# Optimization experiments

Measured on AMD Instinct MI355X. Metric: run time of the kernel, lower is better.

Reference implementation:

```python
import jax, jax.numpy as jnp
import numpy as np

B, LC, LPV, LTP, V, H, NGLO, PREF = 64, 512, 16, 16, 8192, 1024, 30000, 16
BOS = 2
TAU = 0.67
NEG = -1e9


def mask_via_len(lens, max_len):
    # [B,1,max_len] float mask, 1 where pos < len
    return (jnp.arange(max_len)[None, :] < lens[:, None]).astype(jnp.float32)[:, None, :]


def setup_inputs() -> dict:
    key = jax.random.key(0)
    ks = jax.random.split(key, 24)
    s = 0.02
    return {
        "context": jax.random.randint(ks[0], (B, LC), 0, NGLO),
        "context_len": jax.random.randint(ks[1], (B,), 1, LC),
        "pv_m": jax.random.uniform(ks[2], (B, LPV, V), dtype=jnp.float32),
        "pv_m_mask": jnp.ones((B, 1, LPV), jnp.float32),
        "ar_gth": jax.random.randint(ks[3], (B, 1), 0, V),
        "ar_gth_len": jnp.ones((B,), jnp.int64 if jax.config.jax_enable_x64 else jnp.int32),
        "tp_path": jax.random.randint(ks[4], (B, LTP), 0, V),
        "tp_path_len": jax.random.randint(ks[5], (B,), 1, LTP),
        "tp_path_hidden": jax.random.normal(ks[6], (B, LTP, H), jnp.float32),
        "ar_hidden": jax.random.normal(ks[7], (B, 1, H), jnp.float32),
        # learned parameters
        "E_ctx": jax.random.normal(ks[8], (NGLO, H), jnp.float32) * s,
        "W_p": jax.random.normal(ks[9], (V, H), jnp.float32) * s,
        "E_topic": jax.random.normal(ks[10], (V, H), jnp.float32) * s,
        "W_q": jax.random.normal(ks[11], (H, H), jnp.float32) * s,
        "W_k": jax.random.normal(ks[12], (H, H), jnp.float32) * s,
        "W_v": jax.random.normal(ks[13], (H, H), jnp.float32) * s,
        "W_o": jax.random.normal(ks[14], (H, H), jnp.float32) * s,
        "gen_W": jax.random.normal(ks[15], (H, V), jnp.float32) * s,
        "gen_b": jnp.zeros((V,), jnp.float32),
        "glo2loc": jax.random.randint(ks[16], (NGLO,), 0, V),
    }


def _decode(seq_gumbel, src_hidden, src_mask, E_topic, W_q, W_k, W_v, W_o):
    # single-step cross-attention decoder stand-in; dec_out [B,1,H]
    emb = seq_gumbel[:, -1:, :] @ E_topic                      # [B,1,H]
    q = emb @ W_q
    k = src_hidden @ W_k
    v = src_hidden @ W_v
    s = jnp.einsum("bqh,bsh->bqs", q, k) * (H ** -0.5)
    s = jnp.where(src_mask == 0, NEG, s)                       # src_mask [B,1,Ls]
    a = jax.nn.softmax(s, axis=-1)
    ctx = jnp.einsum("bqs,bsh->bqh", a, v)
    return jnp.tanh((emb + ctx) @ W_o)


def _proj(dec_out, src_hidden, src_mask, pv_m, transfer_ctx, tp_oh, gen_W, gen_b):
    # dec_out [B,1,H]
    bsz = dec_out.shape[0]
    gen_logit = dec_out @ gen_W + gen_b                        # [B,1,V]
    hid = src_hidden[:, :-1, :]
    msk = src_mask[:, :, :-1]                                  # [B,1,Ls-1]
    copy_logit = jnp.einsum("bqh,bsh->bqs", dec_out, hid)
    copy_logit = jnp.where(msk == 0, NEG, copy_logit)
    logits = jnp.concatenate([gen_logit, copy_logit], -1) * (H ** -0.5)  # scale_prj
    probs = jax.nn.softmax(logits, axis=-1)
    gen_prob = probs[:, :, :V]
    copy_ctx_p = probs[:, :, V:V + LC]
    copy_pv_p = probs[:, :, V + LC:V + LC + LPV] @ pv_m        # [B,1,V]
    copy_tp_p = probs[:, :, V + LC + LPV:V + LC + LPV + LTP] @ tp_oh
    # scatter-add context copy mass into local topic vocab
    ccopy = jnp.zeros((bsz, 1, V), probs.dtype)
    ccopy = ccopy.at[jnp.arange(bsz)[:, None, None], 0, transfer_ctx[:, None, :]].add(copy_ctx_p)
    return gen_prob + copy_pv_p + copy_tp_p + ccopy


def reference(context, context_len, pv_m, pv_m_mask, ar_gth, ar_gth_len, tp_path,
              tp_path_len, tp_path_hidden, ar_hidden, E_ctx, W_p, E_topic,
              W_q, W_k, W_v, W_o, gen_W, gen_b, glo2loc):
    ar_mask = mask_via_len(ar_gth_len, 1)
    ctx_mask = mask_via_len(context_len, LC)
    ctx_hidden = E_ctx[context] * jnp.swapaxes(ctx_mask, 1, 2)  # masked-embedding encoder
    pv_hidden = jnp.einsum("blv,vh->blh", pv_m, W_p)            # p_encoder stand-in
    tp_oh = jax.nn.one_hot(tp_path, V, dtype=jnp.float32)
    tp_mask = mask_via_len(tp_path_len, LTP)
    src_hidden = jnp.concatenate([ctx_hidden, pv_hidden, tp_path_hidden, ar_hidden], 1)
    src_mask = jnp.concatenate([ctx_mask, pv_m_mask, tp_mask, ar_mask], 2)
    transfer_ctx = glo2loc[context]                             # [B,LC] -> topic vocab ids

    seq = jax.nn.one_hot(jnp.full((pv_m.shape[0], 1), BOS), V, dtype=jnp.float32)
    probs_steps = []
    gkey = jax.random.key(42)
    for t in range(PREF):
        dec = _decode(jax.lax.stop_gradient(seq), src_hidden, src_mask,
                      E_topic, W_q, W_k, W_v, W_o)
        p = _proj(dec, src_hidden, src_mask, pv_m, transfer_ctx, tp_oh, gen_W, gen_b)
        # gumbel-softmax on normed probs
        u = jax.random.uniform(jax.random.fold_in(gkey, t), p.shape, minval=1e-10, maxval=1.0)
        g = -jnp.log(-jnp.log(u))
        y = jax.nn.softmax((jnp.log(p + 1e-10) + g) / TAU, axis=-1)
        probs_steps.append(p)
        seq = jnp.concatenate([seq, y], 1)
    seq_gen_prob = jnp.concatenate(probs_steps, 1)              # [B,PREF,V]
    return seq_gen_prob, seq[:, 1:, :]
```

## Files before the change

kernel.cpp:

```cpp
#include <hip/hip_runtime.h>
#include <hip/hip_bf16.h>
#include <stdint.h>

#define B_    64
#define LC_   512
#define V_    8192
#define H_    1024
#define PREF_ 16
#define S_    545
#define SP_   560
#define NEGV  (-1e9f)
#define INV32 0.03125f

typedef __attribute__((ext_vector_type(8))) short s8v;
typedef __attribute__((ext_vector_type(4))) float f4a;

__device__ __forceinline__ short f2bf(float f){
  uint32_t u = __float_as_uint(f);
  uint32_t r = (u + 0x7fffu + ((u >> 16) & 1u)) >> 16;
  return (short)(r & 0xffffu);
}
__device__ __forceinline__ float bf2f(short s){
  return __uint_as_float(((uint32_t)(uint16_t)s) << 16);
}

__device__ __forceinline__ uint32_t rotl32(uint32_t x, uint32_t d){ return (x<<d)|(x>>(32u-d)); }
__device__ __forceinline__ void tf2x32(uint32_t k0, uint32_t k1, uint32_t& x0, uint32_t& x1){
  uint32_t ks0=k0, ks1=k1, ks2=k0^k1^0x1BD11BDAu;
  x0+=ks0; x1+=ks1;
  x0+=x1; x1=rotl32(x1,13); x1^=x0;
  x0+=x1; x1=rotl32(x1,15); x1^=x0;
  x0+=x1; x1=rotl32(x1,26); x1^=x0;
  x0+=x1; x1=rotl32(x1, 6); x1^=x0;
  x0+=ks1; x1+=ks2+1u;
  x0+=x1; x1=rotl32(x1,17); x1^=x0;
  x0+=x1; x1=rotl32(x1,29); x1^=x0;
  x0+=x1; x1=rotl32(x1,16); x1^=x0;
  x0+=x1; x1=rotl32(x1,24); x1^=x0;
  x0+=ks2; x1+=ks0+2u;
  x0+=x1; x1=rotl32(x1,13); x1^=x0;
  x0+=x1; x1=rotl32(x1,15); x1^=x0;
  x0+=x1; x1=rotl32(x1,26); x1^=x0;
  x0+=x1; x1=rotl32(x1, 6); x1^=x0;
  x0+=ks0; x1+=ks1+3u;
  x0+=x1; x1=rotl32(x1,17); x1^=x0;
  x0+=x1; x1=rotl32(x1,29); x1^=x0;
  x0+=x1; x1=rotl32(x1,16); x1^=x0;
  x0+=x1; x1=rotl32(x1,24); x1^=x0;
  x0+=ks1; x1+=ks2+4u;
  x0+=x1; x1=rotl32(x1,13); x1^=x0;
  x0+=x1; x1=rotl32(x1,15); x1^=x0;
  x0+=x1; x1=rotl32(x1,26); x1^=x0;
  x0+=x1; x1=rotl32(x1, 6); x1^=x0;
  x0+=ks2; x1+=ks0+5u;
}

__global__ __launch_bounds__(256) void cast_bf(const float* __restrict__ in, short* __restrict__ out){
  size_t idx = ((size_t)blockIdx.x*256 + threadIdx.x)*4;
  float4 v = *(const float4*)(in+idx);
  short4 s; s.x=f2bf(v.x); s.y=f2bf(v.y); s.z=f2bf(v.z); s.w=f2bf(v.w);
  *(short4*)(out+idx) = s;
}
__global__ __launch_bounds__(256) void cast_pack(const float* __restrict__ in, short* __restrict__ out, int N){
  int gid = blockIdx.x*256 + threadIdx.x;
  int k = gid / (N>>2);
  int n = (gid % (N>>2))*4;
  float4 v = *(const float4*)(in + (size_t)k*N + n);
  size_t base = ((size_t)(k>>3)*N + n)*8 + (k&7);
  out[base] = f2bf(v.x); out[base+8] = f2bf(v.y); out[base+16] = f2bf(v.z); out[base+24] = f2bf(v.w);
}
__global__ __launch_bounds__(256) void embcast(const float* __restrict__ emb, short* __restrict__ EA){
  int idx = blockIdx.x*256 + threadIdx.x;
  int row = idx >> 8, c4 = idx & 255;
  float4 v = ((const float4*)(emb + (size_t)row*1024))[c4];
  short4 s; s.x=f2bf(v.x); s.y=f2bf(v.y); s.z=f2bf(v.z); s.w=f2bf(v.w);
  *(short4*)(EA + (size_t)row*2048 + c4*4) = s;
}

template<int BM, bool ATOMIC, bool BIAS>
__global__ __launch_bounds__(256) void bgemm(
    const short* __restrict__ A, int lda,
    const short* __restrict__ Bp, int ldn,
    float* __restrict__ C, int ldc,
    int kchunk, const float* __restrict__ bias)
{
  constexpr int BN = 128, BK = 64;
  __shared__ short Bl[BK*BN];
  const int t = threadIdx.x;
  const int w = t >> 6, lane = t & 63;
  const int quad = lane >> 4, l16 = lane & 15;
  const int col0 = blockIdx.x * BN;
  const int row0 = (BM==128) ? blockIdx.y * BM : 0;
  const int k0 = blockIdx.z * kchunk, kend = k0 + kchunk;
  constexpr int MT = 2;
  constexpr int NT = (BM==128) ? 8 : 4;
  const int mbase = (BM==128) ? w*32 : (w&1)*32;
  const int nbase = (BM==128) ? 0 : (w>>1)*64;
  f4a acc[MT][NT];
  #pragma unroll
  for (int mt=0; mt<MT; mt++)
    #pragma unroll
    for (int nt=0; nt<NT; nt++)
      acc[mt][nt] = (f4a){0.f,0.f,0.f,0.f};

  for (int kb = k0; kb < kend; kb += BK){
    #pragma unroll
    for (int i=0;i<4;i++){
      int idx = t + i*256;
      int p = idx >> 7, n = idx & 127;
      ((s8v*)Bl)[idx] = *(const s8v*)(Bp + (((size_t)((kb>>3)+p))*ldn + col0 + n)*8);
    }
    __syncthreads();
    #pragma unroll
    for (int ks=0; ks<BK; ks+=32){
      const int kk = kb + ks + quad*8;
      const int kl = ks + quad*8;
      s8v af[MT], bfr[NT];
      #pragma unroll
      for (int mt=0; mt<MT; mt++)
        af[mt] = *(const s8v*)(A + (size_t)(row0+mbase+mt*16+l16)*lda + kk);
      #pragma unroll
      for (int nt=0; nt<NT; nt++)
        bfr[nt] = *(const s8v*)&Bl[((kl>>3)*BN + nbase + nt*16 + l16)*8];
      #pragma unroll
      for (int mt=0; mt<MT; mt++)
        #pragma unroll
        for (int nt=0; nt<NT; nt++)
          acc[mt][nt] = __builtin_amdgcn_mfma_f32_16x16x32_bf16(af[mt], bfr[nt], acc[mt][nt], 0, 0, 0);
    }
    __syncthreads();
  }
  #pragma unroll
  for (int mt=0; mt<MT; mt++){
    #pragma unroll
    for (int nt=0; nt<NT; nt++){
      #pragma unroll
      for (int r=0; r<4; r++){
        int row = row0 + mbase + mt*16 + quad*4 + r;
        int cc  = col0 + nbase + nt*16 + l16;
        float v = acc[mt][nt][r];
        if (BIAS){ if (!ATOMIC || blockIdx.z==0) v += bias[cc]; }
        size_t idx = (size_t)row*ldc + cc;
        if (ATOMIC) atomicAdd(&C[idx], v);
        else        C[idx] = v;
      }
    }
  }
}

template<bool TRANSB, bool PACK>
__global__ __launch_bounds__(256) void mgemm(
    const float* __restrict__ A, int lda,
    const float* __restrict__ Bm, int ldb,
    float* __restrict__ C, int ldc, int K)
{
  constexpr int BM = 128, BN = 128, BK = 64;
  __shared__ short Ap[BK*BM];
  __shared__ short Bp[BK*BN];
  const int t = threadIdx.x;
  const int w = t >> 6, lane = t & 63;
  const int quad = lane >> 4, l16 = lane & 15;
  const int col0 = blockIdx.x * BN;
  const int row0 = blockIdx.y * BM;
  constexpr int MT = 2, NT = 8;
  const int mbase = w*32, nbase = 0;
  f4a acc[MT][NT];
  #pragma unroll
  for (int mt=0; mt<MT; mt++)
    #pragma unroll
    for (int nt=0; nt<NT; nt++)
      acc[mt][nt] = (f4a){0.f,0.f,0.f,0.f};

  for (int kb = 0; kb < K; kb += BK){
    #pragma unroll
    for (int i = 0; i < 8; ++i){
      int idx = t + i*256;
      int m = idx >> 4, kq = (idx & 15) * 4;
      float4 a = *(const float4*)(A + (size_t)(row0+m)*lda + kb + kq);
      short4 s4; s4.x=f2bf(a.x); s4.y=f2bf(a.y); s4.z=f2bf(a.z); s4.w=f2bf(a.w);
      *(short4*)&Ap[((kq>>3)*BM + m)*8 + (kq&7)] = s4;
    }
    if (TRANSB){
      #pragma unroll
      for (int i = 0; i < 8; ++i){
        int idx = t + i*256;
        int n = idx >> 4, kq = (idx & 15) * 4;
        float4 bv = *(const float4*)(Bm + (size_t)(col0+n)*ldb + kb + kq);
        short4 s4; s4.x=f2bf(bv.x); s4.y=f2bf(bv.y); s4.z=f2bf(bv.z); s4.w=f2bf(bv.w);
        *(short4*)&Bp[((kq>>3)*BN + n)*8 + (kq&7)] = s4;
      }
    } else {
      #pragma unroll
      for (int c = 0; c < 8; ++c){
        int idx = t + c*256;
        int n = idx & 127, kq = (idx >> 7) * 4;
        const float* bp0 = Bm + (size_t)(kb+kq)*ldb + col0 + n;
        float b0 = bp0[0], b1 = bp0[ldb], b2 = bp0[2*(size_t)ldb], b3 = bp0[3*(size_t)ldb];
        short4 s4; s4.x=f2bf(b0); s4.y=f2bf(b1); s4.z=f2bf(b2); s4.w=f2bf(b3);
        *(short4*)&Bp[((kq>>3)*BN + n)*8 + (kq&7)] = s4;
      }
    }
    __syncthreads();
    #pragma unroll
    for (int ks = 0; ks < BK; ks += 32){
      const int kk = ks + quad*8;
      s8v af[MT], bfr[NT];
      #pragma unroll
      for (int mt=0; mt<MT; mt++)
        af[mt] = *(const s8v*)&Ap[((kk>>3)*BM + mbase + mt*16 + l16)*8];
      #pragma unroll
      for (int nt=0; nt<NT; nt++)
        bfr[nt] = *(const s8v*)&Bp[((kk>>3)*BN + nbase + nt*16 + l16)*8];
      #pragma unroll
      for (int mt=0; mt<MT; mt++)
        #pragma unroll
        for (int nt=0; nt<NT; nt++)
          acc[mt][nt] = __builtin_amdgcn_mfma_f32_16x16x32_bf16(af[mt], bfr[nt], acc[mt][nt], 0, 0, 0);
    }
    __syncthreads();
  }
  #pragma unroll
  for (int mt=0; mt<MT; mt++){
    #pragma unroll
    for (int nt=0; nt<NT; nt++){
      #pragma unroll
      for (int r=0; r<4; r++){
        int row = row0 + mbase + mt*16 + quad*4 + r;
        int cc  = col0 + nbase + nt*16 + l16;
        float v = acc[mt][nt][r];
        if (PACK){
          size_t off = (((size_t)(row>>3))*ldc + cc)*8 + (row&7);
          ((short*)C)[off] = f2bf(v);
        } else {
          C[(size_t)row*ldc + cc] = v;
        }
      }
    }
  }
}

__global__ __launch_bounds__(256) void src_build(
    const float* __restrict__ E_ctx, const int* __restrict__ context, const int* __restrict__ ctx_len,
    const float* __restrict__ pvh, const float* __restrict__ pv_mask,
    const float* __restrict__ tp_hidden, const int* __restrict__ tp_len,
    const float* __restrict__ ar_hidden, const int* __restrict__ ar_len,
    short* __restrict__ src, float* __restrict__ smask)
{
  const int b = blockIdx.x, t = threadIdx.x;
  const int j = blockIdx.y*2 + (t >> 7);
  const int c = (t & 127) * 8;
  const float* srcp = nullptr;
  float msk = 0.f;
  if (j < 512){
    bool on = j < ctx_len[b];
    msk = on ? 1.f : 0.f;
    if (on) srcp = E_ctx + (size_t)context[b*LC_ + j]*H_;
  } else if (j < 528){
    srcp = pvh + (size_t)(b*16 + j-512)*H_;
    msk = pv_mask[b*16 + j-512];
  } else if (j < 544){
    srcp = tp_hidden + (size_t)(b*16 + j-528)*H_;
    msk = ((j-528) < tp_len[b]) ? 1.f : 0.f;
  } else if (j == 544){
    srcp = ar_hidden + (size_t)b*H_;
    msk = (ar_len[b] > 0) ? 1.f : 0.f;
  }
  if (srcp){
    float4 v0 = *(const float4*)(srcp + c);
    float4 v1 = *(const float4*)(srcp + c + 4);
    s8v s;
    s[0]=f2bf(v0.x); s[1]=f2bf(v0.y); s[2]=f2bf(v0.z); s[3]=f2bf(v0.w);
    s[4]=f2bf(v1.x); s[5]=f2bf(v1.y); s[6]=f2bf(v1.z); s[7]=f2bf(v1.w);
    *(s8v*)(src + (size_t)(b*SP_ + j)*H_ + c) = s;
  }
  if ((t & 127) == 0) smask[b*SP_ + j] = msk;
}

__global__ __launch_bounds__(256) void abuf_init(short* __restrict__ Abuf){
  int v = blockIdx.x*256 + threadIdx.x;
  int b = blockIdx.y;
  Abuf[(size_t)b*V_ + v] = (v == 2) ? (short)0x3F80 : (short)0;
}

__global__ __launch_bounds__(256) void attn_pass(
    const float* __restrict__ qk, const short* __restrict__ src, const float* __restrict__ smask,
    float* __restrict__ part_o, float* __restrict__ part_ml)
{
  const int b = blockIdx.x, c = blockIdx.y, t = threadIdx.x;
  const int w = t>>6, lane = t&63;
  __shared__ float sv[35], pr[35], red[4];
  float qreg[16];
  {
    const float4* q4 = (const float4*)(qk + (size_t)b*H_ + lane*16);
    #pragma unroll
    for (int i=0;i<4;i++){ float4 v = q4[i]; qreg[4*i]=v.x; qreg[4*i+1]=v.y; qreg[4*i+2]=v.z; qreg[4*i+3]=v.w; }
  }
  const int j0 = c*35;
  for (int r = w; r < 35; r += 4){
    float msk = smask[b*SP_ + j0 + r];
    float s = -3.4e38f;
    if (msk != 0.f){
      const s8v* rp = (const s8v*)(src + (size_t)(b*SP_ + j0 + r)*H_);
      s8v v0 = rp[lane*2], v1 = rp[lane*2+1];
      float acc = 0.f;
      #pragma unroll
      for (int i=0;i<8;i++) acc += bf2f(v0[i])*qreg[i];
      #pragma unroll
      for (int i=0;i<8;i++) acc += bf2f(v1[i])*qreg[8+i];
      #pragma unroll
      for (int off=32; off; off>>=1) acc += __shfl_down(acc, off, 64);
      s = acc * INV32;
    }
    if (lane == 0) sv[r] = s;
  }
  __syncthreads();
  float lm = (t < 35) ? sv[t] : -3.4e38f;
  #pragma unroll
  for (int off=32; off; off>>=1) lm = fmaxf(lm, __shfl_down(lm, off, 64));
  if (lane==0) red[w] = lm;
  __syncthreads();
  const float m = fmaxf(fmaxf(red[0],red[1]), fmaxf(red[2],red[3]));
  __syncthreads();
  if (t < 35) pr[t] = (sv[t] > -1e37f) ? expf(sv[t]-m) : 0.f;
  __syncthreads();
  float ls = (t < 35) ? pr[t] : 0.f;
  #pragma unroll
  for (int off=32; off; off>>=1) ls += __shfl_down(ls, off, 64);
  if (lane==0) red[w] = ls;
  __syncthreads();
  const float lsum = red[0]+red[1]+red[2]+red[3];
  float4 o = {0.f,0.f,0.f,0.f};
  const short* base = src + (size_t)(b*SP_ + j0)*H_ + t*4;
  for (int r=0;r<35;r++){
    float p_ = pr[r];
    if (p_ != 0.f){
      short4 s4 = *(const short4*)(base + (size_t)r*H_);
      o.x += p_*bf2f(s4.x); o.y += p_*bf2f(s4.y); o.z += p_*bf2f(s4.z); o.w += p_*bf2f(s4.w);
    }
  }
  ((float4*)(part_o + (size_t)(b*16+c)*H_))[t] = o;
  if (t==0){ part_ml[(b*16+c)*2] = m; part_ml[(b*16+c)*2+1] = lsum; }
}

__global__ __launch_bounds__(256) void attn_combine(
    const float* __restrict__ part_o, const float* __restrict__ part_ml,
    short* __restrict__ EA)
{
  const int b = blockIdx.x, t = threadIdx.x;
  __shared__ float sm[16], sl[16];
  if (t < 16){ sm[t] = part_ml[(b*16+t)*2]; sl[t] = part_ml[(b*16+t)*2+1]; }
  __syncthreads();
  float M = -3.4e38f;
  #pragma unroll
  for (int i=0;i<16;i++) M = fmaxf(M, sm[i]);
  float wgt[16]; float Z = 0.f;
  #pragma unroll
  for (int i=0;i<16;i++){ wgt[i] = expf(sm[i]-M); Z += wgt[i]*sl[i]; }
  float4 o = {0.f,0.f,0.f,0.f};
  #pragma unroll
  for (int i=0;i<16;i++){
    float4 p = ((const float4*)(part_o + (size_t)(b*16+i)*H_))[t];
    o.x += wgt[i]*p.x; o.y += wgt[i]*p.y; o.z += wgt[i]*p.z; o.w += wgt[i]*p.w;
  }
  float inv = 1.f / Z;
  short4 s4; s4.x=f2bf(o.x*inv); s4.y=f2bf(o.y*inv); s4.z=f2bf(o.z*inv); s4.w=f2bf(o.w*inv);
  *(short4*)(EA + (size_t)b*2048 + 1024 + t*4) = s4;
}

__global__ __launch_bounds__(256) void tanhcast(const float* __restrict__ decr, short* __restrict__ dtan){
  int idx = blockIdx.x*256 + threadIdx.x;
  float4 v = ((const float4*)decr)[idx];
  short4 s; s.x=f2bf(tanhf(v.x)); s.y=f2bf(tanhf(v.y)); s.z=f2bf(tanhf(v.z)); s.w=f2bf(tanhf(v.w));
  ((short4*)dtan)[idx] = s;
}

__global__ __launch_bounds__(256) void copy_score(
    const short* __restrict__ dtan, const short* __restrict__ src, const float* __restrict__ smask,
    float* __restrict__ cl)
{
  const int b = blockIdx.x, c = blockIdx.y, t = threadIdx.x;
  const int w = t>>6, lane = t&63;
  float qd[16];
  {
    const s8v* d8 = (const s8v*)(dtan + (size_t)b*H_ + lane*16);
    s8v d0 = d8[0], d1 = d8[1];
    #pragma unroll
    for (int i=0;i<8;i++){ qd[i] = bf2f(d0[i]); qd[8+i] = bf2f(d1[i]); }
  }
  for (int r = w; r < 34; r += 4){
    int j = c*34 + r;
    float msk = smask[b*SP_ + j];
    float s;
    if (msk != 0.f){
      const s8v* rp = (const s8v*)(src + (size_t)(b*SP_ + j)*H_);
      s8v v0 = rp[lane*2], v1 = rp[lane*2+1];
      float acc = 0.f;
      #pragma unroll
      for (int i=0;i<8;i++) acc += bf2f(v0[i])*qd[i];
      #pragma unroll
      for (int i=0;i<8;i++) acc += bf2f(v1[i])*qd[8+i];
      #pragma unroll
      for (int off=32; off; off>>=1) acc += __shfl_down(acc, off, 64);
      s = acc * INV32;
    } else s = NEGV * INV32;
    if (lane == 0) cl[b*544 + j] = s;
  }
}

__global__ __launch_bounds__(1024) void fuse_out(
    const float* __restrict__ gen, const float* __restrict__ cl, const float* __restrict__ pv_m,
    const int* __restrict__ context, const int* __restrict__ glo2loc, const int* __restrict__ tp_path,
    float* __restrict__ out0, float* __restrict__ out1, short* __restrict__ Abuf, int step)
{
  const int b = blockIdx.x, t = threadIdx.x;
  const int w = t>>6, lane = t&63;
  __shared__ float pl[V_];
  __shared__ float red[16];
  __shared__ float pvp[16];
  float4 gv[2];
  const float4* g4 = (const float4*)(gen + (size_t)b*V_);
  float lm = -3.4e38f;
  #pragma unroll
  for (int i=0;i<2;i++){
    float4 g = g4[t + 1024*i];
    g.x*=INV32; g.y*=INV32; g.z*=INV32; g.w*=INV32;
    gv[i] = g;
    lm = fmaxf(lm, fmaxf(fmaxf(g.x,g.y), fmaxf(g.z,g.w)));
  }
  if (t < 544) lm = fmaxf(lm, cl[b*544+t]);
  #pragma unroll
  for (int off=32; off; off>>=1) lm = fmaxf(lm, __shfl_down(lm, off, 64));
  if (lane==0) red[w] = lm;
  __syncthreads();
  float m = red[0];
  #pragma unroll
  for (int i=1;i<16;i++) m = fmaxf(m, red[i]);
  __syncthreads();
  float ls = 0.f;
  #pragma unroll
  for (int i=0;i<2;i++){
    gv[i].x = expf(gv[i].x - m); gv[i].y = expf(gv[i].y - m);
    gv[i].z = expf(gv[i].z - m); gv[i].w = expf(gv[i].w - m);
    ls += gv[i].x + gv[i].y + gv[i].z + gv[i].w;
  }
  if (t < 544) ls += expf(cl[b*544+t] - m);
  #pragma unroll
  for (int off=32; off; off>>=1) ls += __shfl_down(ls, off, 64);
  if (lane==0) red[w] = ls;
  __syncthreads();
  float Z = red[0];
  #pragma unroll
  for (int i=1;i<16;i++) Z += red[i];
  const float invZ = 1.f / Z;
  if (t < 16) pvp[t] = expf(cl[b*544 + 512 + t] - m) * invZ;
  __syncthreads();
  #pragma unroll
  for (int i=0;i<2;i++){ gv[i].x*=invZ; gv[i].y*=invZ; gv[i].z*=invZ; gv[i].w*=invZ; }
  for (int l=0;l<16;l++){
    float wl = pvp[l];
    const float4* pv4 = (const float4*)(pv_m + (size_t)(b*16+l)*V_);
    #pragma unroll
    for (int i=0;i<2;i++){
      float4 q = pv4[t + 1024*i];
      gv[i].x += wl*q.x; gv[i].y += wl*q.y; gv[i].z += wl*q.z; gv[i].w += wl*q.w;
    }
  }
  #pragma unroll
  for (int i=0;i<2;i++) ((float4*)pl)[t + 1024*i] = gv[i];
  __syncthreads();
  if (t < 528){
    float val; int tgt;
    if (t < 512){
      val = expf(cl[b*544 + t] - m) * invZ;
      tgt = glo2loc[context[b*LC_ + t]];
    } else {
      int l = t - 512;
      val = expf(cl[b*544 + 528 + l] - m) * invZ;
      tgt = tp_path[b*16 + l];
    }
    if (val != 0.f) atomicAdd(&pl[tgt], val);
  }
  __syncthreads();
  float* o0 = out0 + (size_t)(b*PREF_+step)*V_;
  uint32_t kx = 0u, ky = (uint32_t)step;
  tf2x32(0u, 42u, kx, ky);
  float lv[8];
  float lm2 = -3.4e38f;
  #pragma unroll
  for (int i=0;i<2;i++){
    float4 p4 = ((const float4*)pl)[t + 1024*i];
    ((float4*)o0)[t + 1024*i] = p4;
    float pe[4] = {p4.x, p4.y, p4.z, p4.w};
    #pragma unroll
    for (int k=0;k<4;k++){
      int v = 4*(t + 1024*i) + k;
      uint32_t j = (uint32_t)(b*V_ + v);
      uint32_t x0 = 0u, x1 = j;
      tf2x32(kx, ky, x0, x1);
      uint32_t bits = x0 ^ x1;
      float f = __uint_as_float((bits >> 9) | 0x3F800000u) - 1.0f;
      float u = fmaxf(1e-10f, f + 1e-10f);
      float g = -logf(-logf(u));
      float l = (logf(pe[k] + 1e-10f) + g) / 0.67f;
      lv[4*i+k] = l;
      lm2 = fmaxf(lm2, l);
    }
  }
  #pragma unroll
  for (int off=32; off; off>>=1) lm2 = fmaxf(lm2, __shfl_down(lm2, off, 64));
  if (lane==0) red[w] = lm2;
  __syncthreads();
  float m2 = red[0];
  #pragma unroll
  for (int i=1;i<16;i++) m2 = fmaxf(m2, red[i]);
  __syncthreads();
  float ls2 = 0.f;
  #pragma unroll
  for (int i=0;i<8;i++){ lv[i] = expf(lv[i] - m2); ls2 += lv[i]; }
  #pragma unroll
  for (int off=32; off; off>>=1) ls2 += __shfl_down(ls2, off, 64);
  if (lane==0) red[w] = ls2;
  __syncthreads();
  float Z2 = red[0];
  #pragma unroll
  for (int i=1;i<16;i++) Z2 += red[i];
  float* y = out1 + (size_t)(b*PREF_ + step)*V_;
  short* ab = Abuf + (size_t)b*V_;
  #pragma unroll
  for (int i=0;i<2;i++){
    float4 y4; y4.x = lv[4*i]/Z2; y4.y = lv[4*i+1]/Z2; y4.z = lv[4*i+2]/Z2; y4.w = lv[4*i+3]/Z2;
    ((float4*)y)[t + 1024*i] = y4;
    short4 s4; s4.x=f2bf(y4.x); s4.y=f2bf(y4.y); s4.z=f2bf(y4.z); s4.w=f2bf(y4.w);
    *(short4*)(ab + 4*(t + 1024*i)) = s4;
  }
}

extern "C" void kernel_launch(void* const* d_in, const int* in_sizes, int n_in,
                              void* d_out, int out_size, void* d_ws, size_t ws_size,
                              hipStream_t stream)
{
  (void)in_sizes; (void)n_in; (void)out_size; (void)ws_size;
  const int*   context   = (const int*)  d_in[0];
  const int*   ctx_len   = (const int*)  d_in[1];
  const float* pv_m      = (const float*)d_in[2];
  const float* pv_mask   = (const float*)d_in[3];
  const int*   ar_len    = (const int*)  d_in[5];
  const int*   tp_path   = (const int*)  d_in[6];
  const int*   tp_len    = (const int*)  d_in[7];
  const float* tp_hidden = (const float*)d_in[8];
  const float* ar_hidden = (const float*)d_in[9];
  const float* E_ctx     = (const float*)d_in[10];
  const float* W_p       = (const float*)d_in[11];
  const float* E_topic   = (const float*)d_in[12];
  const float* W_q       = (const float*)d_in[13];
  const float* W_k       = (const float*)d_in[14];
  const float* W_v       = (const float*)d_in[15];
  const float* W_o       = (const float*)d_in[16];
  const float* gen_W     = (const float*)d_in[17];
  const float* gen_b     = (const float*)d_in[18];
  const int*   glo2loc   = (const int*)  d_in[19];

  float* out0 = (float*)d_out;
  float* out1 = out0 + (size_t)B_*PREF_*V_;

  short* sw      = (short*)d_ws;
  short* Etp_pk  = sw;  sw += (size_t)8192*1024;
  short* genW_pk = sw;  sw += (size_t)1024*8192;
  short* WoV_pk  = sw;  sw += (size_t)2048*1024;
  short* Mw_pk   = sw;  sw += (size_t)1024*1024;
  short* Abuf    = sw;  sw += (size_t)B_*V_;
  short* EA      = sw;  sw += (size_t)B_*2048;
  short* dtan    = sw;  sw += (size_t)B_*H_;
  short* src_bf  = sw;  sw += (size_t)B_*SP_*H_;
  short* pvm_bf  = src_bf;
  short* Wp_pk   = src_bf + (size_t)1024*8192;
  float* fw      = (float*)sw;
  float* smask   = fw;  fw += B_*SP_;
  float* pvh     = fw;  fw += 1024*1024;
  float* emb     = fw;  fw += B_*H_;
  float* qk      = fw;  fw += B_*H_;
  float* decr    = fw;  fw += B_*H_;
  float* gen     = fw;  fw += (size_t)B_*V_;
  float* part_o  = fw;  fw += (size_t)B_*16*H_;
  float* part_ml = fw;  fw += B_*16*2;
  float* cl      = fw;  fw += B_*544;
  const size_t zbytes = (size_t)(3*B_*H_) * sizeof(float);

  hipMemsetAsync(pvh, 0, (size_t)1024*1024*sizeof(float), stream);
  cast_bf  <<<dim3(8192), dim3(256), 0, stream>>>(pv_m, pvm_bf);
  cast_pack<<<dim3(8192), dim3(256), 0, stream>>>(W_p, Wp_pk, 1024);
  bgemm<128,true,false><<<dim3(8,8,4), dim3(256), 0, stream>>>(
      pvm_bf, 8192, Wp_pk, 1024, pvh, 1024, 2048, nullptr);
  mgemm<true,true><<<dim3(8,8,1), dim3(256), 0, stream>>>(
      W_q, H_, W_k, H_, (float*)Mw_pk, H_, H_);
  cast_pack<<<dim3(1024), dim3(256), 0, stream>>>(W_o, WoV_pk, 1024);
  mgemm<false,true><<<dim3(8,8,1), dim3(256), 0, stream>>>(
      W_v, H_, W_o, H_, (float*)(WoV_pk + (size_t)1024*1024), H_, H_);
  cast_pack<<<dim3(8192), dim3(256), 0, stream>>>(E_topic, Etp_pk, 1024);
  cast_pack<<<dim3(8192), dim3(256), 0, stream>>>(gen_W, genW_pk, 8192);
  src_build<<<dim3(64,280), dim3(256), 0, stream>>>(
      E_ctx, context, ctx_len, pvh, pv_mask, tp_hidden, tp_len, ar_hidden, ar_len, src_bf, smask);
  abuf_init<<<dim3(32,64), dim3(256), 0, stream>>>(Abuf);

  for (int t = 0; t < PREF_; ++t){
    hipMemsetAsync(emb, 0, zbytes, stream);
    bgemm<64,true,false><<<dim3(8,1,16), dim3(256), 0, stream>>>(
        Abuf, V_, Etp_pk, H_, emb, H_, 512, nullptr);
    embcast<<<dim3(64), dim3(256), 0, stream>>>(emb, EA);
    bgemm<64,true,false><<<dim3(8,1,2), dim3(256), 0, stream>>>(
        EA, 2048, Mw_pk, H_, qk, H_, 512, nullptr);
    attn_pass<<<dim3(64,16), dim3(256), 0, stream>>>(qk, src_bf, smask, part_o, part_ml);
    attn_combine<<<dim3(64), dim3(256), 0, stream>>>(part_o, part_ml, EA);
    bgemm<64,true,false><<<dim3(8,1,4), dim3(256), 0, stream>>>(
        EA, 2048, WoV_pk, H_, decr, H_, 512, nullptr);
    tanhcast<<<dim3(64), dim3(256), 0, stream>>>(decr, dtan);
    bgemm<64,false,true><<<dim3(64,1,1), dim3(256), 0, stream>>>(
        dtan, H_, genW_pk, V_, gen, V_, 1024, gen_b);
    copy_score<<<dim3(64,16), dim3(256), 0, stream>>>(dtan, src_bf, smask, cl);
    fuse_out<<<dim3(64), dim3(1024), 0, stream>>>(
        gen, cl, pv_m, context, glo2loc, tp_path, out0, out1, Abuf, t);
  }
}
```

Baseline: 2.720 ms.

## Double-buffer bgemm B tiles, replace mgemm with bf16 bgemm, read bf16 pv_m

The bgemm kernel now double-buffers its shared-memory B tile, loading the next K tile while computing the current one. The fp32 mgemm weight-fusion GEMMs are replaced by bf16 casts followed by split-K bgemm with a repack step. The per-step Mw and WoV GEMVs get more K splits. fuse_out now reads the bf16 pv_m copy kept in its own buffer instead of fp32 pv_m, with 8 contiguous elements per thread. This trades extra shared memory, more atomics and a bit of bf16 precision loss in the pv mixture for less memory traffic and better latency hiding.

Result: faster. 2.217 ms (-18.5%).

```diff
diff --git a/kernel.cpp b/kernel.cpp
--- a/kernel.cpp
+++ b/kernel.cpp
@@ -69,6 +69,15 @@
   size_t base = ((size_t)(k>>3)*N + n)*8 + (k&7);
   out[base] = f2bf(v.x); out[base+8] = f2bf(v.y); out[base+16] = f2bf(v.z); out[base+24] = f2bf(v.w);
 }
+__global__ __launch_bounds__(256) void cast_packT(const float* __restrict__ in, short* __restrict__ out, int N, int K){
+  int gid = blockIdx.x*256 + threadIdx.x;
+  int n = gid / (K>>2);
+  int k = (gid % (K>>2))*4;
+  float4 v = *(const float4*)(in + (size_t)n*K + k);
+  size_t base = ((size_t)(k>>3)*N + n)*8 + (k&7);
+  short4 s4; s4.x=f2bf(v.x); s4.y=f2bf(v.y); s4.z=f2bf(v.z); s4.w=f2bf(v.w);
+  *(short4*)(out + base) = s4;
+}
 __global__ __launch_bounds__(256) void embcast(const float* __restrict__ emb, short* __restrict__ EA){
   int idx = blockIdx.x*256 + threadIdx.x;
   int row = idx >> 8, c4 = idx & 255;
@@ -85,13 +94,14 @@
     int kchunk, const float* __restrict__ bias)
 {
   constexpr int BN = 128, BK = 64;
-  __shared__ short Bl[BK*BN];
+  __shared__ short Bl[2][BK*BN];
   const int t = threadIdx.x;
   const int w = t >> 6, lane = t & 63;
   const int quad = lane >> 4, l16 = lane & 15;
   const int col0 = blockIdx.x * BN;
   const int row0 = (BM==128) ? blockIdx.y * BM : 0;
-  const int k0 = blockIdx.z * kchunk, kend = k0 + kchunk;
+  const int k0 = blockIdx.z * kchunk;
+  const int nk = kchunk / BK;
   constexpr int MT = 2;
   constexpr int NT = (BM==128) ? 8 : 4;
   const int mbase = (BM==128) ? w*32 : (w&1)*32;
@@ -103,14 +113,21 @@
     for (int nt=0; nt<NT; nt++)
       acc[mt][nt] = (f4a){0.f,0.f,0.f,0.f};
 
-  for (int kb = k0; kb < kend; kb += BK){
+  auto stage = [&](int kb, int buf){
     #pragma unroll
     for (int i=0;i<4;i++){
       int idx = t + i*256;
       int p = idx >> 7, n = idx & 127;
-      ((s8v*)Bl)[idx] = *(const s8v*)(Bp + (((size_t)((kb>>3)+p))*ldn + col0 + n)*8);
-    }
-    __syncthreads();
+      ((s8v*)Bl[buf])[idx] = *(const s8v*)(Bp + (((size_t)((kb>>3)+p))*ldn + col0 + n)*8);
+    }
+  };
+
+  stage(k0, 0);
+  __syncthreads();
+  for (int it=0; it<nk; ++it){
+    const int kb = k0 + it*BK;
+    const int cur = it & 1;
+    if (it+1 < nk) stage(kb + BK, cur^1);
     #pragma unroll
     for (int ks=0; ks<BK; ks+=32){
       const int kk = kb + ks + quad*8;
@@ -121,7 +138,7 @@
         af[mt] = *(const s8v*)(A + (size_t)(row0+mbase+mt*16+l16)*lda + kk);
       #pragma unroll
       for (int nt=0; nt<NT; nt++)
-        bfr[nt] = *(const s8v*)&Bl[((kl>>3)*BN + nbase + nt*16 + l16)*8];
+        bfr[nt] = *(const s8v*)&Bl[cur][((kl>>3)*BN + nbase + nt*16 + l16)*8];
       #pragma unroll
       for (int mt=0; mt<MT; mt++)
         #pragma unroll
@@ -143,97 +160,6 @@
         size_t idx = (size_t)row*ldc + cc;
         if (ATOMIC) atomicAdd(&C[idx], v);
         else        C[idx] = v;
-      }
-    }
-  }
-}
-
-template<bool TRANSB, bool PACK>
-__global__ __launch_bounds__(256) void mgemm(
-    const float* __restrict__ A, int lda,
-    const float* __restrict__ Bm, int ldb,
-    float* __restrict__ C, int ldc, int K)
-{
-  constexpr int BM = 128, BN = 128, BK = 64;
-  __shared__ short Ap[BK*BM];
-  __shared__ short Bp[BK*BN];
-  const int t = threadIdx.x;
-  const int w = t >> 6, lane = t & 63;
-  const int quad = lane >> 4, l16 = lane & 15;
-  const int col0 = blockIdx.x * BN;
-  const int row0 = blockIdx.y * BM;
-  constexpr int MT = 2, NT = 8;
-  const int mbase = w*32, nbase = 0;
-  f4a acc[MT][NT];
-  #pragma unroll
-  for (int mt=0; mt<MT; mt++)
-    #pragma unroll
-    for (int nt=0; nt<NT; nt++)
-      acc[mt][nt] = (f4a){0.f,0.f,0.f,0.f};
-
-  for (int kb = 0; kb < K; kb += BK){
-    #pragma unroll
-    for (int i = 0; i < 8; ++i){
-      int idx = t + i*256;
-      int m = idx >> 4, kq = (idx & 15) * 4;
-      float4 a = *(const float4*)(A + (size_t)(row0+m)*lda + kb + kq);
-      short4 s4; s4.x=f2bf(a.x); s4.y=f2bf(a.y); s4.z=f2bf(a.z); s4.w=f2bf(a.w);
-      *(short4*)&Ap[((kq>>3)*BM + m)*8 + (kq&7)] = s4;
-    }
-    if (TRANSB){
-      #pragma unroll
-      for (int i = 0; i < 8; ++i){
-        int idx = t + i*256;
-        int n = idx >> 4, kq = (idx & 15) * 4;
-        float4 bv = *(const float4*)(Bm + (size_t)(col0+n)*ldb + kb + kq);
-        short4 s4; s4.x=f2bf(bv.x); s4.y=f2bf(bv.y); s4.z=f2bf(bv.z); s4.w=f2bf(bv.w);
-        *(short4*)&Bp[((kq>>3)*BN + n)*8 + (kq&7)] = s4;
-      }
-    } else {
-      #pragma unroll
-      for (int c = 0; c < 8; ++c){
-        int idx = t + c*256;
-        int n = idx & 127, kq = (idx >> 7) * 4;
-        const float* bp0 = Bm + (size_t)(kb+kq)*ldb + col0 + n;
-        float b0 = bp0[0], b1 = bp0[ldb], b2 = bp0[2*(size_t)ldb], b3 = bp0[3*(size_t)ldb];
-        short4 s4; s4.x=f2bf(b0); s4.y=f2bf(b1); s4.z=f2bf(b2); s4.w=f2bf(b3);
-        *(short4*)&Bp[((kq>>3)*BN + n)*8 + (kq&7)] = s4;
-      }
-    }
-    __syncthreads();
-    #pragma unroll
-    for (int ks = 0; ks < BK; ks += 32){
-      const int kk = ks + quad*8;
-      s8v af[MT], bfr[NT];
-      #pragma unroll
-      for (int mt=0; mt<MT; mt++)
-        af[mt] = *(const s8v*)&Ap[((kk>>3)*BM + mbase + mt*16 + l16)*8];
-      #pragma unroll
-      for (int nt=0; nt<NT; nt++)
-        bfr[nt] = *(const s8v*)&Bp[((kk>>3)*BN + nbase + nt*16 + l16)*8];
-      #pragma unroll
-      for (int mt=0; mt<MT; mt++)
-        #pragma unroll
-        for (int nt=0; nt<NT; nt++)
-          acc[mt][nt] = __builtin_amdgcn_mfma_f32_16x16x32_bf16(af[mt], bfr[nt], acc[mt][nt], 0, 0, 0);
-    }
-    __syncthreads();
-  }
-  #pragma unroll
-  for (int mt=0; mt<MT; mt++){
-    #pragma unroll
-    for (int nt=0; nt<NT; nt++){
-      #pragma unroll
-      for (int r=0; r<4; r++){
-        int row = row0 + mbase + mt*16 + quad*4 + r;
-        int cc  = col0 + nbase + nt*16 + l16;
-        float v = acc[mt][nt][r];
-        if (PACK){
-          size_t off = (((size_t)(row>>3))*ldc + cc)*8 + (row&7);
-          ((short*)C)[off] = f2bf(v);
-        } else {
-          C[(size_t)row*ldc + cc] = v;
-        }
       }
     }
   }
@@ -408,7 +334,7 @@
 }
 
 __global__ __launch_bounds__(1024) void fuse_out(
-    const float* __restrict__ gen, const float* __restrict__ cl, const float* __restrict__ pv_m,
+    const float* __restrict__ gen, const float* __restrict__ cl, const short* __restrict__ pvm,
     const int* __restrict__ context, const int* __restrict__ glo2loc, const int* __restrict__ tp_path,
     float* __restrict__ out0, float* __restrict__ out1, short* __restrict__ Abuf, int step)
 {
@@ -417,15 +343,15 @@
   __shared__ float pl[V_];
   __shared__ float red[16];
   __shared__ float pvp[16];
-  float4 gv[2];
+  float ge[8];
   const float4* g4 = (const float4*)(gen + (size_t)b*V_);
   float lm = -3.4e38f;
-  #pragma unroll
-  for (int i=0;i<2;i++){
-    float4 g = g4[t + 1024*i];
-    g.x*=INV32; g.y*=INV32; g.z*=INV32; g.w*=INV32;
-    gv[i] = g;
-    lm = fmaxf(lm, fmaxf(fmaxf(g.x,g.y), fmaxf(g.z,g.w)));
+  {
+    float4 ga = g4[2*t], gb = g4[2*t+1];
+    ge[0]=ga.x*INV32; ge[1]=ga.y*INV32; ge[2]=ga.z*INV32; ge[3]=ga.w*INV32;
+    ge[4]=gb.x*INV32; ge[5]=gb.y*INV32; ge[6]=gb.z*INV32; ge[7]=gb.w*INV32;
+    #pragma unroll
+    for (int k=0;k<8;k++) lm = fmaxf(lm, ge[k]);
   }
   if (t < 544) lm = fmaxf(lm, cl[b*544+t]);
   #pragma unroll
@@ -438,11 +364,7 @@
   __syncthreads();
   float ls = 0.f;
   #pragma unroll
-  for (int i=0;i<2;i++){
-    gv[i].x = expf(gv[i].x - m); gv[i].y = expf(gv[i].y - m);
-    gv[i].z = expf(gv[i].z - m); gv[i].w = expf(gv[i].w - m);
-    ls += gv[i].x + gv[i].y + gv[i].z + gv[i].w;
-  }
+  for (int k=0;k<8;k++){ ge[k] = expf(ge[k] - m); ls += ge[k]; }
   if (t < 544) ls += expf(cl[b*544+t] - m);
   #pragma unroll
   for (int off=32; off; off>>=1) ls += __shfl_down(ls, off, 64);
@@ -455,18 +377,19 @@
   if (t < 16) pvp[t] = expf(cl[b*544 + 512 + t] - m) * invZ;
   __syncthreads();
   #pragma unroll
-  for (int i=0;i<2;i++){ gv[i].x*=invZ; gv[i].y*=invZ; gv[i].z*=invZ; gv[i].w*=invZ; }
+  for (int k=0;k<8;k++) ge[k] *= invZ;
+  const short* pvb = pvm + (size_t)b*16*V_ + 8*t;
+  #pragma unroll 4
   for (int l=0;l<16;l++){
     float wl = pvp[l];
-    const float4* pv4 = (const float4*)(pv_m + (size_t)(b*16+l)*V_);
-    #pragma unroll
-    for (int i=0;i<2;i++){
-      float4 q = pv4[t + 1024*i];
-      gv[i].x += wl*q.x; gv[i].y += wl*q.y; gv[i].z += wl*q.z; gv[i].w += wl*q.w;
-    }
-  }
-  #pragma unroll
-  for (int i=0;i<2;i++) ((float4*)pl)[t + 1024*i] = gv[i];
+    s8v q = *(const s8v*)(pvb + (size_t)l*V_);
+    #pragma unroll
+    for (int k=0;k<8;k++) ge[k] += wl*bf2f(q[k]);
+  }
+  {
+    float4 pa = {ge[0],ge[1],ge[2],ge[3]}, pb = {ge[4],ge[5],ge[6],ge[7]};
+    ((float4*)pl)[2*t] = pa; ((float4*)pl)[2*t+1] = pb;
+  }
   __syncthreads();
   if (t < 528){
     float val; int tgt;
@@ -486,14 +409,13 @@
   tf2x32(0u, 42u, kx, ky);
   float lv[8];
   float lm2 = -3.4e38f;
-  #pragma unroll
-  for (int i=0;i<2;i++){
-    float4 p4 = ((const float4*)pl)[t + 1024*i];
-    ((float4*)o0)[t + 1024*i] = p4;
-    float pe[4] = {p4.x, p4.y, p4.z, p4.w};
-    #pragma unroll
-    for (int k=0;k<4;k++){
-      int v = 4*(t + 1024*i) + k;
+  {
+    float4 pa = ((const float4*)pl)[2*t], pb = ((const float4*)pl)[2*t+1];
+    ((float4*)o0)[2*t] = pa; ((float4*)o0)[2*t+1] = pb;
+    float pe[8] = {pa.x,pa.y,pa.z,pa.w, pb.x,pb.y,pb.z,pb.w};
+    #pragma unroll
+    for (int k=0;k<8;k++){
+      int v = 8*t + k;
       uint32_t j = (uint32_t)(b*V_ + v);
       uint32_t x0 = 0u, x1 = j;
       tf2x32(kx, ky, x0, x1);
@@ -502,7 +424,7 @@
       float u = fmaxf(1e-10f, f + 1e-10f);
       float g = -logf(-logf(u));
       float l = (logf(pe[k] + 1e-10f) + g) / 0.67f;
-      lv[4*i+k] = l;
+      lv[k] = l;
       lm2 = fmaxf(lm2, l);
     }
   }
@@ -516,7 +438,7 @@
   __syncthreads();
   float ls2 = 0.f;
   #pragma unroll
-  for (int i=0;i<8;i++){ lv[i] = expf(lv[i] - m2); ls2 += lv[i]; }
+  for (int k=0;k<8;k++){ lv[k] = expf(lv[k] - m2); ls2 += lv[k]; }
   #pragma unroll
   for (int off=32; off; off>>=1) ls2 += __shfl_down(ls2, off, 64);
   if (lane==0) red[w] = ls2;
@@ -526,12 +448,14 @@
   for (int i=1;i<16;i++) Z2 += red[i];
   float* y = out1 + (size_t)(b*PREF_ + step)*V_;
   short* ab = Abuf + (size_t)b*V_;
-  #pragma unroll
-  for (int i=0;i<2;i++){
-    float4 y4; y4.x = lv[4*i]/Z2; y4.y = lv[4*i+1]/Z2; y4.z = lv[4*i+2]/Z2; y4.w = lv[4*i+3]/Z2;
-    ((float4*)y)[t + 1024*i] = y4;
-    short4 s4; s4.x=f2bf(y4.x); s4.y=f2bf(y4.y); s4.z=f2bf(y4.z); s4.w=f2bf(y4.w);
-    *(short4*)(ab + 4*(t + 1024*i)) = s4;
+  {
+    float4 y4a; y4a.x = lv[0]/Z2; y4a.y = lv[1]/Z2; y4a.z = lv[2]/Z2; y4a.w = lv[3]/Z2;
+    float4 y4b; y4b.x = lv[4]/Z2; y4b.y = lv[5]/Z2; y4b.z = lv[6]/Z2; y4b.w = lv[7]/Z2;
+    ((float4*)y)[2*t] = y4a; ((float4*)y)[2*t+1] = y4b;
+    s8v s;
+    s[0]=f2bf(y4a.x); s[1]=f2bf(y4a.y); s[2]=f2bf(y4a.z); s[3]=f2bf(y4a.w);
+    s[4]=f2bf(y4b.x); s[5]=f2bf(y4b.y); s[6]=f2bf(y4b.z); s[7]=f2bf(y4b.w);
+    *(s8v*)(ab + 8*t) = s;
   }
 }
 
@@ -568,12 +492,15 @@
   short* genW_pk = sw;  sw += (size_t)1024*8192;
   short* WoV_pk  = sw;  sw += (size_t)2048*1024;
   short* Mw_pk   = sw;  sw += (size_t)1024*1024;
+  short* pvm_bf  = sw;  sw += (size_t)1024*8192;
   short* Abuf    = sw;  sw += (size_t)B_*V_;
   short* EA      = sw;  sw += (size_t)B_*2048;
   short* dtan    = sw;  sw += (size_t)B_*H_;
   short* src_bf  = sw;  sw += (size_t)B_*SP_*H_;
-  short* pvm_bf  = src_bf;
-  short* Wp_pk   = src_bf + (size_t)1024*8192;
+  short* Wp_pk   = src_bf;
+  short* wq_bf   = src_bf + (size_t)8192*1024;
+  short* wv_bf   = wq_bf  + (size_t)1024*1024;
+  short* WkT_pk  = wv_bf  + (size_t)1024*1024;
   float* fw      = (float*)sw;
   float* smask   = fw;  fw += B_*SP_;
   float* pvh     = fw;  fw += 1024*1024;
@@ -585,17 +512,26 @@
   float* part_ml = fw;  fw += B_*16*2;
   float* cl      = fw;  fw += B_*544;
   const size_t zbytes = (size_t)(3*B_*H_) * sizeof(float);
-
+  float* Mw_f  = pvh;
+  float* Wvo_f = part_o;
+
+  hipMemsetAsync(Mw_f,  0, (size_t)1024*1024*sizeof(float), stream);
+  hipMemsetAsync(Wvo_f, 0, (size_t)1024*1024*sizeof(float), stream);
+  cast_bf   <<<dim3(1024), dim3(256), 0, stream>>>(W_q, wq_bf);
+  cast_packT<<<dim3(1024), dim3(256), 0, stream>>>(W_k, WkT_pk, 1024, 1024);
+  cast_bf   <<<dim3(1024), dim3(256), 0, stream>>>(W_v, wv_bf);
+  cast_pack <<<dim3(1024), dim3(256), 0, stream>>>(W_o, WoV_pk, 1024);
+  bgemm<128,true,false><<<dim3(8,8,4), dim3(256), 0, stream>>>(
+      wq_bf, 1024, WkT_pk, 1024, Mw_f, 1024, 256, nullptr);
+  cast_pack <<<dim3(1024), dim3(256), 0, stream>>>(Mw_f, Mw_pk, 1024);
+  bgemm<128,true,false><<<dim3(8,8,4), dim3(256), 0, stream>>>(
+      wv_bf, 1024, WoV_pk, 1024, Wvo_f, 1024, 256, nullptr);
+  cast_pack <<<dim3(1024), dim3(256), 0, stream>>>(Wvo_f, WoV_pk + (size_t)1024*1024, 1024);
   hipMemsetAsync(pvh, 0, (size_t)1024*1024*sizeof(float), stream);
   cast_bf  <<<dim3(8192), dim3(256), 0, stream>>>(pv_m, pvm_bf);
   cast_pack<<<dim3(8192), dim3(256), 0, stream>>>(W_p, Wp_pk, 1024);
   bgemm<128,true,false><<<dim3(8,8,4), dim3(256), 0, stream>>>(
       pvm_bf, 8192, Wp_pk, 1024, pvh, 1024, 2048, nullptr);
-  mgemm<true,true><<<dim3(8,8,1), dim3(256), 0, stream>>>(
-      W_q, H_, W_k, H_, (float*)Mw_pk, H_, H_);
-  cast_pack<<<dim3(1024), dim3(256), 0, stream>>>(W_o, WoV_pk, 1024);
-  mgemm<false,true><<<dim3(8,8,1), dim3(256), 0, stream>>>(
-      W_v, H_, W_o, H_, (float*)(WoV_pk + (size_t)1024*1024), H_, H_);
   cast_pack<<<dim3(8192), dim3(256), 0, stream>>>(E_topic, Etp_pk, 1024);
   cast_pack<<<dim3(8192), dim3(256), 0, stream>>>(gen_W, genW_pk, 8192);
   src_build<<<dim3(64,280), dim3(256), 0, stream>>>(
@@ -607,17 +543,17 @@
     bgemm<64,true,false><<<dim3(8,1,16), dim3(256), 0, stream>>>(
         Abuf, V_, Etp_pk, H_, emb, H_, 512, nullptr);
     embcast<<<dim3(64), dim3(256), 0, stream>>>(emb, EA);
-    bgemm<64,true,false><<<dim3(8,1,2), dim3(256), 0, stream>>>(
-        EA, 2048, Mw_pk, H_, qk, H_, 512, nullptr);
+    bgemm<64,true,false><<<dim3(8,1,8), dim3(256), 0, stream>>>(
+        EA, 2048, Mw_pk, H_, qk, H_, 128, nullptr);
     attn_pass<<<dim3(64,16), dim3(256), 0, stream>>>(qk, src_bf, smask, part_o, part_ml);
     attn_combine<<<dim3(64), dim3(256), 0, stream>>>(part_o, part_ml, EA);
-    bgemm<64,true,false><<<dim3(8,1,4), dim3(256), 0, stream>>>(
-        EA, 2048, WoV_pk, H_, decr, H_, 512, nullptr);
+    bgemm<64,true,false><<<dim3(8,1,8), dim3(256), 0, stream>>>(
+        EA, 2048, WoV_pk, H_, decr, H_, 256, nullptr);
     tanhcast<<<dim3(64), dim3(256), 0, stream>>>(decr, dtan);
     bgemm<64,false,true><<<dim3(64,1,1), dim3(256), 0, stream>>>(
         dtan, H_, genW_pk, V_, gen, V_, 1024, gen_b);
     copy_score<<<dim3(64,16), dim3(256), 0, stream>>>(dtan, src_bf, smask, cl);
     fuse_out<<<dim3(64), dim3(1024), 0, stream>>>(
-        gen, cl, pv_m, context, glo2loc, tp_path, out0, out1, Abuf, t);
-  }
-}
+        gen, cl, pvm_bf, context, glo2loc, tp_path, out0, out1, Abuf, t);
+  }
+}
```
